# Kernel optimization log

Measured on AMD Instinct MI355X. Metric: run time of the kernel, lower is better.

The kernel has to match this reference:

```python
import jax, jax.numpy as jnp
import numpy as np

T, B, D = 2048, 8, 1024
INIT_ALPHA_BIAS = 2.0


def setup_inputs() -> dict:
    key = jax.random.key(0)
    k1, k2, k3, k4 = jax.random.split(key, 4)
    xav = float(np.sqrt(6.0 / (D + D)))  # xavier_uniform bound
    return {
        "x": jax.random.normal(k1, (T, B, D), dtype=jnp.float32),
        "h0": jax.random.normal(k2, (B, D), dtype=jnp.float32),
        "W_alpha": jax.random.uniform(k3, (D, D), jnp.float32, -xav, xav),
        "b_alpha": jnp.full((D,), INIT_ALPHA_BIAS, dtype=jnp.float32),
        "W_v": jax.random.uniform(k4, (D, D), jnp.float32, -xav, xav),
        "b_v": jnp.zeros((D,), dtype=jnp.float32),
    }


def reference(x, h0, W_alpha, b_alpha, W_v, b_v):
    # Gates/values for all timesteps at once (batched GEMMs): [T, B, D]
    alpha = jax.nn.sigmoid(jnp.einsum("tbd,ed->tbe", x, W_alpha) + b_alpha)
    v = jnp.einsum("tbd,ed->tbe", x, W_v) + b_v

    def step(h_prev, av):
        a_t, v_t = av
        h_new = a_t * h_prev + (1.0 - a_t) * v_t
        out_t = h_new * jax.nn.silu(h_new)
        return h_new, (h_new, out_t)

    _, (hs, output) = jax.lax.scan(step, h0, (alpha, v))
    h = jnp.concatenate([h0[None], hs], axis=0)  # [T+1, B, D]
    return output, h
```

## Files before the change

### kernel.cpp

```cpp
#include <hip/hip_runtime.h>
#include <hip/hip_bf16.h>

#define T_DIM 2048
#define B_DIM 8
#define D_DIM 1024
#define M_DIM (T_DIM * B_DIM)
#define K_DIM D_DIM
#define NW_DIM (2 * D_DIM)
#define NCH (B_DIM * D_DIM)
#define NCH4 (NCH / 4)
#define CHUNKS 64
#define CHUNK_LEN 32

typedef __attribute__((ext_vector_type(8))) short bf16x8;
typedef __attribute__((ext_vector_type(4))) float f32x4;

__device__ __forceinline__ unsigned short bf16_rne(float f) {
    unsigned u = __float_as_uint(f);
    unsigned r = u + 0x7fffu + ((u >> 16) & 1u);
    return (unsigned short)(r >> 16);
}

__device__ __forceinline__ float sigmoidf(float z) {
    return 1.0f / (1.0f + __expf(-z));
}

__device__ __forceinline__ void load_lds16(const void* g, void* l) {
    __builtin_amdgcn_global_load_lds(
        (const __attribute__((address_space(1))) void*)g,
        (__attribute__((address_space(3))) void*)l,
        16, 0, 0);
}

__global__ void f32_to_bf16_kernel(const float4* __restrict__ in,
                                   ushort4* __restrict__ out, int n4) {
    int i = blockIdx.x * blockDim.x + threadIdx.x;
    if (i < n4) {
        float4 f = in[i];
        ushort4 o;
        o.x = bf16_rne(f.x);
        o.y = bf16_rne(f.y);
        o.z = bf16_rne(f.z);
        o.w = bf16_rne(f.w);
        out[i] = o;
    }
}

__global__ void conv_weights_kernel(const float4* __restrict__ Wa,
                                    const float4* __restrict__ Wv,
                                    ushort4* __restrict__ Wcat) {
    const int half4 = D_DIM * D_DIM / 4;
    int i = blockIdx.x * blockDim.x + threadIdx.x;
    float4 f = (i < half4) ? Wa[i] : Wv[i - half4];
    ushort4 o;
    o.x = bf16_rne(f.x);
    o.y = bf16_rne(f.y);
    o.z = bf16_rne(f.z);
    o.w = bf16_rne(f.w);
    Wcat[i] = o;
}

__global__ __launch_bounds__(256) void gemm_fused_kernel(
    const unsigned short* __restrict__ A,
    const unsigned short* __restrict__ W,
    const float* __restrict__ ba,
    const float* __restrict__ bv,
    float* __restrict__ alpha_dst,
    float* __restrict__ v_dst) {
    __shared__ __attribute__((aligned(16))) unsigned short As[128 * 64];
    __shared__ __attribute__((aligned(16))) unsigned short Bs[128 * 64];

    const int tid = threadIdx.x;
    const int lane = tid & 63;
    const int w = tid >> 6;
    const int wm = w >> 1;
    const int wn = w & 1;
    const int quad = lane >> 4;
    const int l16 = lane & 15;
    const int xr = l16 & 7;

    const int bm = blockIdx.y * 128;
    const int bn = blockIdx.x * 128;

    const int st_row = lane >> 3;
    const int st_col = ((lane & 7) ^ st_row) * 8;

    f32x4 zero = {0.f, 0.f, 0.f, 0.f};
    f32x4 acc[4][4];
#pragma unroll
    for (int i = 0; i < 4; ++i)
#pragma unroll
        for (int j = 0; j < 4; ++j) acc[i][j] = zero;

    for (int kt = 0; kt < K_DIM / 64; ++kt) {
        const int k0 = kt * 64;
#pragma unroll
        for (int j = 0; j < 4; ++j) {
            const int r = w * 32 + j * 8;
            load_lds16(A + (size_t)(bm + r + st_row) * K_DIM + k0 + st_col,
                       &As[r * 64]);
            load_lds16(W + (size_t)(bn + r + st_row) * K_DIM + k0 + st_col,
                       &Bs[r * 64]);
        }
        __syncthreads();
#pragma unroll
        for (int s = 0; s < 2; ++s) {
            bf16x8 af[4], bfr[4];
#pragma unroll
            for (int i = 0; i < 4; ++i)
                af[i] = *(const bf16x8*)&As[(wm * 64 + i * 16 + l16) * 64 +
                                            (((s * 4 + quad) ^ xr) * 8)];
#pragma unroll
            for (int i = 0; i < 4; ++i)
                bfr[i] = *(const bf16x8*)&Bs[(wn * 64 + i * 16 + l16) * 64 +
                                             (((s * 4 + quad) ^ xr) * 8)];
#pragma unroll
            for (int i = 0; i < 4; ++i)
#pragma unroll
                for (int j = 0; j < 4; ++j)
                    acc[i][j] = __builtin_amdgcn_mfma_f32_16x16x32_bf16(
                        af[i], bfr[j], acc[i][j], 0, 0, 0);
        }
        __syncthreads();
    }

    const bool is_alpha = (bn < D_DIM);
    float* __restrict__ dst = is_alpha ? alpha_dst : v_dst;
    const float* __restrict__ bias = is_alpha ? ba : bv;
    const int nb = bn - (is_alpha ? 0 : D_DIM);
#pragma unroll
    for (int j = 0; j < 4; ++j) {
        const int n = nb + wn * 64 + j * 16 + l16;
        const float bias_n = bias[n];
#pragma unroll
        for (int i = 0; i < 4; ++i) {
            const int m0 = bm + wm * 64 + i * 16 + quad * 4;
#pragma unroll
            for (int r = 0; r < 4; ++r) {
                float val = acc[i][j][r] + bias_n;
                if (is_alpha) val = sigmoidf(val);
                dst[(size_t)(m0 + r) * D_DIM + n] = val;
            }
        }
    }
}


__global__ __launch_bounds__(256) void scan_phase1_kernel(
    const float4* __restrict__ alpha,
    const float4* __restrict__ v,
    float4* __restrict__ P,
    float4* __restrict__ Q) {
    const int j4 = blockIdx.x * 256 + threadIdx.x;
    const int c = blockIdx.y;
    float4 Pr = {1.f, 1.f, 1.f, 1.f};
    float4 Qr = {0.f, 0.f, 0.f, 0.f};
    size_t base = (size_t)c * CHUNK_LEN * NCH4 + j4;
#pragma unroll 4
    for (int t = 0; t < CHUNK_LEN; ++t) {
        float4 a = alpha[base + (size_t)t * NCH4];
        float4 vv = v[base + (size_t)t * NCH4];
        Pr.x *= a.x; Pr.y *= a.y; Pr.z *= a.z; Pr.w *= a.w;
        Qr.x = a.x * Qr.x + (1.f - a.x) * vv.x;
        Qr.y = a.y * Qr.y + (1.f - a.y) * vv.y;
        Qr.z = a.z * Qr.z + (1.f - a.z) * vv.z;
        Qr.w = a.w * Qr.w + (1.f - a.w) * vv.w;
    }
    P[(size_t)c * NCH4 + j4] = Pr;
    Q[(size_t)c * NCH4 + j4] = Qr;
}

__global__ __launch_bounds__(256) void scan_phase2_kernel(
    const float4* __restrict__ P, const float4* __restrict__ Q,
    const float4* __restrict__ h0,
    float4* __restrict__ Hc) {
    const int j4 = blockIdx.x * 256 + threadIdx.x;
    float4 h = h0[j4];
#pragma unroll 8
    for (int c = 0; c < CHUNKS; ++c) {
        Hc[(size_t)c * NCH4 + j4] = h;
        float4 p = P[(size_t)c * NCH4 + j4];
        float4 q = Q[(size_t)c * NCH4 + j4];
        h.x = p.x * h.x + q.x;
        h.y = p.y * h.y + q.y;
        h.z = p.z * h.z + q.z;
        h.w = p.w * h.w + q.w;
    }
}

__global__ __launch_bounds__(256) void scan_phase3_kernel(
    float4* __restrict__ alpha_out,
    float4* __restrict__ v_h,
    const float4* __restrict__ Hc) {
    const int j4 = blockIdx.x * 256 + threadIdx.x;
    const int c = blockIdx.y;
    float4 h = Hc[(size_t)c * NCH4 + j4];
    size_t base = (size_t)c * CHUNK_LEN * NCH4 + j4;
#pragma unroll 4
    for (int t = 0; t < CHUNK_LEN; ++t) {
        float4 a = alpha_out[base + (size_t)t * NCH4];
        float4 vv = v_h[base + (size_t)t * NCH4];
        h.x = a.x * h.x + (1.f - a.x) * vv.x;
        h.y = a.y * h.y + (1.f - a.y) * vv.y;
        h.z = a.z * h.z + (1.f - a.z) * vv.z;
        h.w = a.w * h.w + (1.f - a.w) * vv.w;
        float4 o;
        o.x = h.x * h.x * sigmoidf(h.x);
        o.y = h.y * h.y * sigmoidf(h.y);
        o.z = h.z * h.z * sigmoidf(h.z);
        o.w = h.w * h.w * sigmoidf(h.w);
        alpha_out[base + (size_t)t * NCH4] = o;
        v_h[base + (size_t)t * NCH4] = h;
    }
}

extern "C" void kernel_launch(void* const* d_in, const int* in_sizes, int n_in,
                              void* d_out, int out_size, void* d_ws, size_t ws_size,
                              hipStream_t stream) {
    const float* x  = (const float*)d_in[0];
    const float* h0 = (const float*)d_in[1];
    const float* Wa = (const float*)d_in[2];
    const float* ba = (const float*)d_in[3];
    const float* Wv = (const float*)d_in[4];
    const float* bv = (const float*)d_in[5];

    float* out = (float*)d_out;
    float* hbase = out + (size_t)T_DIM * NCH;
    float* alpha = out;
    float* vbuf = hbase + NCH;

    char* ws = (char*)d_ws;
    unsigned short* xb   = (unsigned short*)ws;
    unsigned short* Wcat = (unsigned short*)(ws + 33554432);
    float* P  = (float*)(ws + 37748736);
    float* Q  = (float*)(ws + 39845888);
    float* Hc = (float*)(ws + 41943040);

    f32_to_bf16_kernel<<<(M_DIM * K_DIM / 4) / 256, 256, 0, stream>>>(
        (const float4*)x, (ushort4*)xb, M_DIM * K_DIM / 4);
    conv_weights_kernel<<<(2 * D_DIM * D_DIM / 4) / 256, 256, 0, stream>>>(
        (const float4*)Wa, (const float4*)Wv, (ushort4*)Wcat);

    dim3 ggrid(NW_DIM / 128, M_DIM / 128);
    gemm_fused_kernel<<<ggrid, 256, 0, stream>>>(xb, Wcat, ba, bv, alpha, vbuf);

    hipMemcpyAsync(hbase, h0, (size_t)NCH * sizeof(float),
                   hipMemcpyDeviceToDevice, stream);

    dim3 sgrid(NCH4 / 256, CHUNKS);
    scan_phase1_kernel<<<sgrid, 256, 0, stream>>>(
        (const float4*)alpha, (const float4*)vbuf, (float4*)P, (float4*)Q);
    scan_phase2_kernel<<<NCH4 / 256, 256, 0, stream>>>(
        (const float4*)P, (const float4*)Q, (const float4*)h0, (float4*)Hc);
    scan_phase3_kernel<<<sgrid, 256, 0, stream>>>(
        (float4*)alpha, (float4*)vbuf, (const float4*)Hc);
}
```

Baseline: 345.1 us.

## Rewrite GEMM with 256x256 tiles, 4-stage LDS pipeline and block swizzle

Replaces the 128x128 single-buffered GEMM with a 256x256-tile, 512-thread kernel that uses a 4-buffer LDS ring (128 KB dynamic shared memory). Loads for tile t+2 are issued while computing tile t, with explicit waitcnt, barriers and setprio around the MFMA phases. A block-index swizzle is added for L2 locality. The aim is to hide global-load latency and raise arithmetic intensity, in exchange for more registers and LDS per block and fragile hand-tuned synchronisation.

```diff
diff --git a/kernel.cpp b/kernel.cpp
--- a/kernel.cpp
+++ b/kernel.cpp
@@ -60,69 +60,130 @@
     Wcat[i] = o;
 }
 
-__global__ __launch_bounds__(256) void gemm_fused_kernel(
+#define MMA_QUAD(IB)                                                        \
+    _Pragma("unroll") for (int i = 0; i < 4; ++i)                           \
+    _Pragma("unroll") for (int j = 0; j < 4; ++j)                           \
+        acc[(IB) + i][j] = __builtin_amdgcn_mfma_f32_16x16x32_bf16(         \
+            af[i], bf[j], acc[(IB) + i][j], 0, 0, 0);
+
+__global__ __launch_bounds__(512, 2) void gemm_fused_kernel(
     const unsigned short* __restrict__ A,
     const unsigned short* __restrict__ W,
     const float* __restrict__ ba,
     const float* __restrict__ bv,
     float* __restrict__ alpha_dst,
     float* __restrict__ v_dst) {
-    __shared__ __attribute__((aligned(16))) unsigned short As[128 * 64];
-    __shared__ __attribute__((aligned(16))) unsigned short Bs[128 * 64];
+    extern __shared__ __attribute__((aligned(16))) char smem[];
 
     const int tid = threadIdx.x;
     const int lane = tid & 63;
     const int w = tid >> 6;
-    const int wm = w >> 1;
-    const int wn = w & 1;
+    const int wm = w >> 2;
+    const int wn = w & 3;
     const int quad = lane >> 4;
     const int l16 = lane & 15;
-    const int xr = l16 & 7;
-
-    const int bm = blockIdx.y * 128;
-    const int bn = blockIdx.x * 128;
-
-    const int st_row = lane >> 3;
-    const int st_col = ((lane & 7) ^ st_row) * 8;
-
-    f32x4 zero = {0.f, 0.f, 0.f, 0.f};
-    f32x4 acc[4][4];
-#pragma unroll
-    for (int i = 0; i < 4; ++i)
-#pragma unroll
-        for (int j = 0; j < 4; ++j) acc[i][j] = zero;
-
-    for (int kt = 0; kt < K_DIM / 64; ++kt) {
-        const int k0 = kt * 64;
-#pragma unroll
-        for (int j = 0; j < 4; ++j) {
-            const int r = w * 32 + j * 8;
-            load_lds16(A + (size_t)(bm + r + st_row) * K_DIM + k0 + st_col,
-                       &As[r * 64]);
-            load_lds16(W + (size_t)(bn + r + st_row) * K_DIM + k0 + st_col,
-                       &Bs[r * 64]);
-        }
-        __syncthreads();
-#pragma unroll
-        for (int s = 0; s < 2; ++s) {
-            bf16x8 af[4], bfr[4];
-#pragma unroll
-            for (int i = 0; i < 4; ++i)
-                af[i] = *(const bf16x8*)&As[(wm * 64 + i * 16 + l16) * 64 +
-                                            (((s * 4 + quad) ^ xr) * 8)];
-#pragma unroll
-            for (int i = 0; i < 4; ++i)
-                bfr[i] = *(const bf16x8*)&Bs[(wn * 64 + i * 16 + l16) * 64 +
-                                             (((s * 4 + quad) ^ xr) * 8)];
-#pragma unroll
-            for (int i = 0; i < 4; ++i)
-#pragma unroll
-                for (int j = 0; j < 4; ++j)
-                    acc[i][j] = __builtin_amdgcn_mfma_f32_16x16x32_bf16(
-                        af[i], bfr[j], acc[i][j], 0, 0, 0);
-        }
-        __syncthreads();
-    }
+
+    const int bid = blockIdx.x;
+    const int swz = (bid & 7) * 64 + (bid >> 3);
+    const int bx = swz & 7;
+    const int by = swz >> 3;
+    const int bm = by * 256;
+    const int bn = bx * 256;
+
+    const int vsw = (((l16 & 1) << 2) | quad) ^ (l16 >> 1);
+    const int rdA = wm * 8192 + (l16 >> 1) * 128 + vsw * 16;
+    const int rdB = wn * 4096 + (l16 >> 1) * 128 + vsw * 16;
+
+    const int p = lane & 7;
+    const int hl = lane >> 3;
+    const int vp = p ^ hl;
+    const int qsrc = vp & 3;
+    const int rb = (vp >> 2) & 1;
+    const int r0 = 16 * (2 * w + 0) + 2 * hl + rb;
+    const int r1 = 16 * (2 * w + 1) + 2 * hl + rb;
+    const char* Ab = (const char*)A;
+    const char* Wb = (const char*)W;
+    const size_t offA0 = (size_t)(bm + r0) * 2048 + (size_t)qsrc * 16;
+    const size_t offA1 = (size_t)(bm + r1) * 2048 + (size_t)qsrc * 16;
+    const size_t offB0 = (size_t)(bn + r0) * 2048 + (size_t)qsrc * 16;
+    const size_t offB1 = (size_t)(bn + r1) * 2048 + (size_t)qsrc * 16;
+    const int lds0 = (2 * w + 0) * 1024;
+    const int lds1 = (2 * w + 1) * 1024;
+
+    f32x4 acc[8][4];
+    bf16x8 af[4], bf[4];
+    {
+        f32x4 zero = {0.f, 0.f, 0.f, 0.f};
+#pragma unroll
+        for (int i = 0; i < 8; ++i)
+#pragma unroll
+            for (int j = 0; j < 4; ++j) acc[i][j] = zero;
+    }
+
+    auto stage_a = [&](int buf, int ts) {
+        char* base = smem + (buf << 15);
+        load_lds16(Ab + offA0 + (size_t)ts * 64, base + lds0);
+        load_lds16(Ab + offA1 + (size_t)ts * 64, base + lds1);
+    };
+    auto stage_b = [&](int buf, int ts) {
+        char* base = smem + (buf << 15) + 16384;
+        load_lds16(Wb + offB0 + (size_t)ts * 64, base + lds0);
+        load_lds16(Wb + offB1 + (size_t)ts * 64, base + lds1);
+    };
+    auto read_a = [&](int buf, int ib) {
+        const char* la = smem + (buf << 15);
+#pragma unroll
+        for (int i = 0; i < 4; ++i)
+            af[i] = *(const bf16x8*)(la + rdA + (ib + i) * 1024);
+    };
+    auto read_b = [&](int buf) {
+        const char* lb = smem + (buf << 15) + 16384;
+#pragma unroll
+        for (int j = 0; j < 4; ++j)
+            bf[j] = *(const bf16x8*)(lb + rdB + j * 1024);
+    };
+
+    auto phaseA = [&](int t, bool do_stage) {
+        const int buf = t & 3;
+        read_a(buf, 0);
+        read_b(buf);
+        if (do_stage) stage_a((t + 2) & 3, t + 2);
+        __builtin_amdgcn_s_barrier();
+        asm volatile("s_waitcnt lgkmcnt(0)" ::: "memory");
+        __builtin_amdgcn_sched_barrier(0);
+        __builtin_amdgcn_s_setprio(1);
+        MMA_QUAD(0)
+        __builtin_amdgcn_s_setprio(0);
+        __builtin_amdgcn_s_barrier();
+    };
+    auto phaseB = [&](int t, bool do_stage, int vm) {
+        const int buf = t & 3;
+        read_a(buf, 4);
+        if (do_stage) stage_b((t + 2) & 3, t + 2);
+        if (vm == 4) asm volatile("s_waitcnt vmcnt(4)" ::: "memory");
+        else if (vm == 0) asm volatile("s_waitcnt vmcnt(0)" ::: "memory");
+        __builtin_amdgcn_s_barrier();
+        asm volatile("s_waitcnt lgkmcnt(0)" ::: "memory");
+        __builtin_amdgcn_sched_barrier(0);
+        __builtin_amdgcn_s_setprio(1);
+        MMA_QUAD(4)
+        __builtin_amdgcn_s_setprio(0);
+        __builtin_amdgcn_s_barrier();
+    };
+
+    stage_a(0, 0); stage_b(0, 0);
+    stage_a(1, 1); stage_b(1, 1);
+    asm volatile("s_waitcnt vmcnt(4)" ::: "memory");
+    __builtin_amdgcn_s_barrier();
+
+    for (int t = 0; t < 30; ++t) {
+        phaseA(t, true);
+        phaseB(t, true, 4);
+    }
+    phaseA(30, false);
+    phaseB(30, false, 0);
+    phaseA(31, false);
+    phaseB(31, false, -1);
 
     const bool is_alpha = (bn < D_DIM);
     float* __restrict__ dst = is_alpha ? alpha_dst : v_dst;
@@ -133,8 +194,8 @@
         const int n = nb + wn * 64 + j * 16 + l16;
         const float bias_n = bias[n];
 #pragma unroll
-        for (int i = 0; i < 4; ++i) {
-            const int m0 = bm + wm * 64 + i * 16 + quad * 4;
+        for (int i = 0; i < 8; ++i) {
+            const int m0 = bm + wm * 128 + i * 16 + quad * 4;
 #pragma unroll
             for (int r = 0; r < 4; ++r) {
                 float val = acc[i][j][r] + bias_n;
@@ -236,13 +297,19 @@
     float* Q  = (float*)(ws + 39845888);
     float* Hc = (float*)(ws + 41943040);
 
+    static bool attr_done = false;
+    if (!attr_done) {
+        hipFuncSetAttribute(reinterpret_cast<const void*>(gemm_fused_kernel),
+                            hipFuncAttributeMaxDynamicSharedMemorySize, 131072);
+        attr_done = true;
+    }
+
     f32_to_bf16_kernel<<<(M_DIM * K_DIM / 4) / 256, 256, 0, stream>>>(
         (const float4*)x, (ushort4*)xb, M_DIM * K_DIM / 4);
     conv_weights_kernel<<<(2 * D_DIM * D_DIM / 4) / 256, 256, 0, stream>>>(
         (const float4*)Wa, (const float4*)Wv, (ushort4*)Wcat);
 
-    dim3 ggrid(NW_DIM / 128, M_DIM / 128);
-    gemm_fused_kernel<<<ggrid, 256, 0, stream>>>(xb, Wcat, ba, bv, alpha, vbuf);
+    gemm_fused_kernel<<<512, 512, 131072, stream>>>(xb, Wcat, ba, bv, alpha, vbuf);
 
     hipMemcpyAsync(hbase, h0, (size_t)NCH * sizeof(float),
                    hipMemcpyDeviceToDevice, stream);
```

New measurement: 327.4 us. 1.05x faster.
